# Kernel tuning notes

Hardware: AMD Instinct MI355X
Metric: run time of the kernel (lower is better)

Reference implementation:

```python
import jax, jax.numpy as jnp
import numpy as np
from jax.ops import segment_sum

N_NODES = 50000
N_EDGES = 800000
IN_DIM, HID_DIM, OUT_DIM = 128, 256, 128


def _glorot(key, shape):
    lim = np.sqrt(6.0 / (shape[0] + shape[1]))
    return jax.random.uniform(key, shape, jnp.float32, -lim, lim)


def setup_inputs() -> dict:
    key = jax.random.key(0)
    ks = jax.random.split(key, 4)
    x = jax.random.normal(ks[0], (N_NODES, IN_DIM), jnp.float32)
    edge_index = jax.random.randint(ks[1], (2, N_EDGES), 0, N_NODES, jnp.int64)
    W1 = _glorot(ks[2], (IN_DIM, HID_DIM))
    b1 = jnp.zeros((HID_DIM,), jnp.float32)
    W2 = _glorot(ks[3], (HID_DIM, OUT_DIM))
    b2 = jnp.zeros((OUT_DIM,), jnp.float32)
    return {"x": x, "edge_index": edge_index, "W1": W1, "b1": b1, "W2": W2, "b2": b2}


def gcn_conv(x, W, b, src, dst, n_nodes):
    # PyG GCNConv: x' = D^{-1/2} (A + I) D^{-1/2} (x W) + b
    h = x @ W  # [N, F_out]
    deg = segment_sum(jnp.ones_like(src, dtype=h.dtype), dst, num_segments=n_nodes) + 1.0  # +1 self loop
    dinv = jax.lax.rsqrt(deg)  # [N]
    norm = dinv[src] * dinv[dst]  # per-edge norm [E]
    msg = h[src] * norm[:, None]  # [E, F_out]
    agg = segment_sum(msg, dst, num_segments=n_nodes)
    agg = agg + h * (dinv * dinv)[:, None]  # self-loop term: norm_ii = dinv_i^2
    return agg + b


def reference(x, edge_index, W1, b1, W2, b2):
    src, dst = edge_index[0], edge_index[1]
    h = gcn_conv(x, W1, b1, src, dst, N_NODES)
    h = jax.nn.relu(h)
    out = gcn_conv(h, W2, b2, src, dst, N_NODES)
    return out
```

## Files before the change

### kernel.cpp

```cpp
#include <hip/hip_runtime.h>

#define N_NODES 50000
#define N_EDGES 800000
#define IN_DIM  128
#define HID_DIM 256
#define OUT_DIM 128
#define BUCKET_CAP 64
#define NCOARSE 196
#define CHUNK 4000
#define NBLK1 200
#define SEGCAP 64
#define HLD 264
#define GROWS 64

typedef __attribute__((ext_vector_type(8))) short short8;
typedef __attribute__((ext_vector_type(4))) float f32x4;

__device__ inline ushort f2b(float f) {
    union { float f; unsigned u; } v; v.f = f;
    return (ushort)((v.u + 0x7FFFu + ((v.u >> 16) & 1u)) >> 16);
}
__device__ inline float b2f(ushort h) {
    union { unsigned u; float f; } v; v.u = ((unsigned)h) << 16;
    return v.f;
}
__device__ inline float2 u2f2(unsigned u) {
    float2 r; r.x = b2f((ushort)(u & 0xFFFFu)); r.y = b2f((ushort)(u >> 16)); return r;
}
__device__ inline unsigned f2u2(float a, float b) {
    return (unsigned)f2b(a) | ((unsigned)f2b(b) << 16);
}
__device__ inline void fma8(float2* acc, uint4 u, float n) {
    float2 v0 = u2f2(u.x), v1 = u2f2(u.y), v2 = u2f2(u.z), v3 = u2f2(u.w);
    acc[0].x += v0.x * n; acc[0].y += v0.y * n;
    acc[1].x += v1.x * n; acc[1].y += v1.y * n;
    acc[2].x += v2.x * n; acc[2].y += v2.y * n;
    acc[3].x += v3.x * n; acc[3].y += v3.y * n;
}


__global__ __launch_bounds__(256) void prep_kernel(const float* __restrict__ x,
                                                   const float* __restrict__ W1,
                                                   const float* __restrict__ W2,
                                                   const int* __restrict__ src,
                                                   const int* __restrict__ dst,
                                                   ushort* __restrict__ xb,
                                                   ushort* __restrict__ w1t,
                                                   ushort* __restrict__ w2t,
                                                   int* __restrict__ bcnt,
                                                   int* __restrict__ binbuf) {
    __shared__ int vals[CHUNK];
    __shared__ ushort lpos[CHUNK];
    __shared__ unsigned char lbin[CHUNK];
    __shared__ int hist[NCOARSE];
    const int b = blockIdx.x;
    const int t = threadIdx.x;
    if (b < 6250) {
        int i = b * 256 + t;
        float4 v = ((const float4*)x)[i];
        ushort4 o; o.x = f2b(v.x); o.y = f2b(v.y); o.z = f2b(v.z); o.w = f2b(v.w);
        ((ushort4*)xb)[i] = o;
    } else if (b < 6506) {
        int i = (b - 6250) * 256 + t;
        if (i < 32768) {
            int n = i >> 7, k = i & 127;
            w1t[i] = f2b(W1[k * HID_DIM + n]);
        } else {
            int j = i - 32768;
            int n = j >> 8, k = j & 255;
            w2t[j] = f2b(W2[k * OUT_DIM + n]);
        }
    } else {
        const int blk = b - 6506;
        const int e0 = blk * CHUNK;
        for (int i = t; i < NCOARSE; i += 256) hist[i] = 0;
        __syncthreads();
        for (int i = t; i < CHUNK; i += 256) {
            int s = src[e0 + i], d = dst[e0 + i];
            int bin = d >> 8;
            vals[i] = (s << 8) | (d & 255);
            lbin[i] = (unsigned char)bin;
            lpos[i] = (ushort)atomicAdd(&hist[bin], 1);
        }
        __syncthreads();
        for (int i = t; i < NCOARSE; i += 256) {
            int h = hist[i]; if (h > SEGCAP) h = SEGCAP;
            bcnt[i * NBLK1 + blk] = h;
        }
        for (int i = t; i < CHUNK; i += 256) {
            int bin = lbin[i];
            int p = lpos[i];
            if (p < SEGCAP) binbuf[((size_t)bin * NBLK1 + blk) * SEGCAP + p] = vals[i];
        }
    }
}


__global__ __launch_bounds__(256) void binpass2_kernel(const int* __restrict__ bcnt,
                                                       const int* __restrict__ binbuf,
                                                       int* __restrict__ cnt,
                                                       float* __restrict__ dinv,
                                                       int* __restrict__ bucket) {
    __shared__ int lcnt[256];
    __shared__ int lm[NBLK1];
    __shared__ int lbuck[256 * BUCKET_CAP];
    const int bin = blockIdx.x;
    const int t = threadIdx.x;
    lcnt[t] = 0;
    if (t < NBLK1) lm[t] = bcnt[bin * NBLK1 + t];
    __syncthreads();
    const int* bb = binbuf + (size_t)bin * NBLK1 * SEGCAP;
    for (int f = t; f < NBLK1 * SEGCAP; f += 256) {
        int blk = f >> 6;
        int sl = f & 63;
        if (sl < lm[blk]) {
            int v = bb[f];
            int dl = v & 255;
            int pos = atomicAdd(&lcnt[dl], 1);
            if (pos < BUCKET_CAP) lbuck[dl * BUCKET_CAP + pos] = v >> 8;
        }
    }
    __syncthreads();
    const int node0 = bin * 256;
    int node = node0 + t;
    if (node < N_NODES) {
        int c = lcnt[t] > BUCKET_CAP ? BUCKET_CAP : lcnt[t];
        cnt[node] = c;
        dinv[node] = rsqrtf((float)c + 1.0f);
    }
    int nvalid = N_NODES - node0; if (nvalid > 256) nvalid = 256;
    if (nvalid <= 0) return;
    int total4 = (nvalid * BUCKET_CAP) >> 2;
    int4* d4 = (int4*)(bucket + (size_t)node0 * BUCKET_CAP);
    const int4* s4 = (const int4*)lbuck;
    for (int j = t; j < total4; j += 256) d4[j] = s4[j];
}


__global__ __launch_bounds__(256) void gather0_kernel(const int* __restrict__ cnt,
                                                      const int* __restrict__ bucket,
                                                      const float* __restrict__ dinv,
                                                      const ushort* __restrict__ xb,
                                                      ushort* __restrict__ aggxb) {
    const int w = blockIdx.x * 4 + (threadIdx.x >> 6);
    const int lane = threadIdx.x & 63;
    const int grp = lane >> 4, sub = lane & 15;
    const int n = cnt[w];
    const float dd = dinv[w];
    int sv = 0; float nv = 0.f;
    if (lane < n) { sv = bucket[w * BUCKET_CAP + lane]; nv = dinv[sv] * dd; }

    float2 acc[4];
    if (grp == 0) {
        uint4 su = ((const uint4*)(xb + (size_t)w * IN_DIM))[sub];
        float sd = dd * dd;
        acc[0] = u2f2(su.x); acc[1] = u2f2(su.y); acc[2] = u2f2(su.z); acc[3] = u2f2(su.w);
#pragma unroll
        for (int j = 0; j < 4; ++j) { acc[j].x *= sd; acc[j].y *= sd; }
    } else {
#pragma unroll
        for (int j = 0; j < 4; ++j) acc[j] = {0.f, 0.f};
    }

    const int nr = (n + 15) & ~15;
    for (int i = 0; i < nr; i += 16) {
        int s0 = __shfl(sv, i + grp),      s1 = __shfl(sv, i + 4 + grp);
        int s2 = __shfl(sv, i + 8 + grp),  s3 = __shfl(sv, i + 12 + grp);
        float n0 = __shfl(nv, i + grp),     n1 = __shfl(nv, i + 4 + grp);
        float n2 = __shfl(nv, i + 8 + grp), n3 = __shfl(nv, i + 12 + grp);
        uint4 u0 = ((const uint4*)(xb + (size_t)s0 * IN_DIM))[sub];
        uint4 u1 = ((const uint4*)(xb + (size_t)s1 * IN_DIM))[sub];
        uint4 u2 = ((const uint4*)(xb + (size_t)s2 * IN_DIM))[sub];
        uint4 u3 = ((const uint4*)(xb + (size_t)s3 * IN_DIM))[sub];
        fma8(acc, u0, n0); fma8(acc, u1, n1); fma8(acc, u2, n2); fma8(acc, u3, n3);
    }
#pragma unroll
    for (int j = 0; j < 4; ++j) {
        acc[j].x += __shfl_down(acc[j].x, 32); acc[j].y += __shfl_down(acc[j].y, 32);
        acc[j].x += __shfl_down(acc[j].x, 16); acc[j].y += __shfl_down(acc[j].y, 16);
    }
    if (lane < 16) {
        uint4 o = {f2u2(acc[0].x, acc[0].y), f2u2(acc[1].x, acc[1].y),
                   f2u2(acc[2].x, acc[2].y), f2u2(acc[3].x, acc[3].y)};
        ((uint4*)(aggxb + (size_t)w * IN_DIM))[sub] = o;
    }
}


__global__ __launch_bounds__(256, 2) void gemm12_mfma(const ushort* __restrict__ aggxb,
                                                      const ushort* __restrict__ w1t,
                                                      const float* __restrict__ b1,
                                                      const ushort* __restrict__ w2t,
                                                      ushort* __restrict__ h2b) {
    __shared__ ushort Hs[GROWS * HLD];
    const int row0 = blockIdx.x * GROWS;
    const int wv = threadIdx.x >> 6;
    const int lane = threadIdx.x & 63;
    const int l15 = lane & 15, q = lane >> 4;

    short8 bf1[16];
#pragma unroll
    for (int kb = 0; kb < 4; ++kb)
#pragma unroll
        for (int t = 0; t < 4; ++t) {
            int col = wv * 64 + t * 16 + l15;
            bf1[kb * 4 + t] = *(const short8*)(w1t + (size_t)col * IN_DIM + kb * 32 + q * 8);
        }
    short8 af[4][4];
#pragma unroll
    for (int sub = 0; sub < 4; ++sub) {
        int ar = row0 + sub * 16 + l15;
        if (ar >= N_NODES) ar = N_NODES - 1;
        const ushort* ab = aggxb + (size_t)ar * IN_DIM + q * 8;
#pragma unroll
        for (int kb = 0; kb < 4; ++kb) af[sub][kb] = *(const short8*)(ab + kb * 32);
    }
    f32x4 acc1[4][4] = {};
#pragma unroll
    for (int sub = 0; sub < 4; ++sub)
#pragma unroll
        for (int kb = 0; kb < 4; ++kb)
#pragma unroll
            for (int t = 0; t < 4; ++t)
                acc1[sub][t] = __builtin_amdgcn_mfma_f32_16x16x32_bf16(
                    af[sub][kb], bf1[kb * 4 + t], acc1[sub][t], 0, 0, 0);
#pragma unroll
    for (int t = 0; t < 4; ++t) {
        int col = wv * 64 + t * 16 + l15;
        float bias = b1[col];
#pragma unroll
        for (int sub = 0; sub < 4; ++sub)
#pragma unroll
            for (int r = 0; r < 4; ++r) {
                int row = sub * 16 + q * 4 + r;
                float v = acc1[sub][t][r] + bias;
                Hs[row * HLD + col] = f2b(v > 0.f ? v : 0.f);
            }
    }
    __syncthreads();

    short8 bf2[16];
#pragma unroll
    for (int kb = 0; kb < 8; ++kb)
#pragma unroll
        for (int t = 0; t < 2; ++t) {
            int col = wv * 32 + t * 16 + l15;
            bf2[kb * 2 + t] = *(const short8*)(w2t + (size_t)col * HID_DIM + kb * 32 + q * 8);
        }
    f32x4 acc2[4][2] = {};
#pragma unroll
    for (int sub = 0; sub < 4; ++sub) {
        const ushort* hb = Hs + (sub * 16 + l15) * HLD + q * 8;
#pragma unroll
        for (int kb = 0; kb < 8; ++kb) {
            short8 a = *(const short8*)(hb + kb * 32);
#pragma unroll
            for (int t = 0; t < 2; ++t)
                acc2[sub][t] = __builtin_amdgcn_mfma_f32_16x16x32_bf16(
                    a, bf2[kb * 2 + t], acc2[sub][t], 0, 0, 0);
        }
    }
#pragma unroll
    for (int sub = 0; sub < 4; ++sub)
#pragma unroll
        for (int t = 0; t < 2; ++t) {
            int col = wv * 32 + t * 16 + l15;
#pragma unroll
            for (int r = 0; r < 4; ++r) {
                int row = row0 + sub * 16 + q * 4 + r;
                if (row < N_NODES)
                    h2b[(size_t)row * OUT_DIM + col] = f2b(acc2[sub][t][r]);
            }
        }
}


__global__ __launch_bounds__(256) void gather2_kernel(const int* __restrict__ cnt,
                                                      const int* __restrict__ bucket,
                                                      const float* __restrict__ dinv,
                                                      const ushort* __restrict__ h2b,
                                                      const float* __restrict__ b2,
                                                      float* __restrict__ out) {
    const int w = blockIdx.x * 4 + (threadIdx.x >> 6);
    const int lane = threadIdx.x & 63;
    const int grp = lane >> 4, sub = lane & 15;
    const int n = cnt[w];
    const float dd = dinv[w];
    int sv = 0; float nv = 0.f;
    if (lane < n) { sv = bucket[w * BUCKET_CAP + lane]; nv = dinv[sv] * dd; }

    float2 acc[4];
    if (grp == 0) {
        uint4 su = ((const uint4*)(h2b + (size_t)w * OUT_DIM))[sub];
        float sd = dd * dd;
        acc[0] = u2f2(su.x); acc[1] = u2f2(su.y); acc[2] = u2f2(su.z); acc[3] = u2f2(su.w);
#pragma unroll
        for (int j = 0; j < 4; ++j) { acc[j].x *= sd; acc[j].y *= sd; }
    } else {
#pragma unroll
        for (int j = 0; j < 4; ++j) acc[j] = {0.f, 0.f};
    }

    const int nr = (n + 15) & ~15;
    for (int i = 0; i < nr; i += 16) {
        int s0 = __shfl(sv, i + grp),      s1 = __shfl(sv, i + 4 + grp);
        int s2 = __shfl(sv, i + 8 + grp),  s3 = __shfl(sv, i + 12 + grp);
        float n0 = __shfl(nv, i + grp),     n1 = __shfl(nv, i + 4 + grp);
        float n2 = __shfl(nv, i + 8 + grp), n3 = __shfl(nv, i + 12 + grp);
        uint4 u0 = ((const uint4*)(h2b + (size_t)s0 * OUT_DIM))[sub];
        uint4 u1 = ((const uint4*)(h2b + (size_t)s1 * OUT_DIM))[sub];
        uint4 u2 = ((const uint4*)(h2b + (size_t)s2 * OUT_DIM))[sub];
        uint4 u3 = ((const uint4*)(h2b + (size_t)s3 * OUT_DIM))[sub];
        fma8(acc, u0, n0); fma8(acc, u1, n1); fma8(acc, u2, n2); fma8(acc, u3, n3);
    }
#pragma unroll
    for (int j = 0; j < 4; ++j) {
        acc[j].x += __shfl_down(acc[j].x, 32); acc[j].y += __shfl_down(acc[j].y, 32);
        acc[j].x += __shfl_down(acc[j].x, 16); acc[j].y += __shfl_down(acc[j].y, 16);
    }
    if (lane < 16) {
        const float4* bp = (const float4*)b2;
        float4 b0 = bp[sub * 2], b1v = bp[sub * 2 + 1];
        float4 o0 = {acc[0].x + b0.x, acc[0].y + b0.y, acc[1].x + b0.z, acc[1].y + b0.w};
        float4 o1 = {acc[2].x + b1v.x, acc[2].y + b1v.y, acc[3].x + b1v.z, acc[3].y + b1v.w};
        float4* op = (float4*)(out + (size_t)w * OUT_DIM);
        op[sub * 2] = o0;
        op[sub * 2 + 1] = o1;
    }
}

extern "C" void kernel_launch(void* const* d_in, const int* in_sizes, int n_in,
                              void* d_out, int out_size, void* d_ws, size_t ws_size,
                              hipStream_t stream) {
    const float* x  = (const float*)d_in[0];
    const int*   ei = (const int*)d_in[1];
    const float* W1 = (const float*)d_in[2];
    const float* b1 = (const float*)d_in[3];
    const float* W2 = (const float*)d_in[4];
    const float* b2 = (const float*)d_in[5];
    float* out = (float*)d_out;

    const int* src = ei;
    const int* dst = ei + N_EDGES;

    char* ws = (char*)d_ws;
    int*    bcnt   = (int*)(ws);
    int*    cnt    = (int*)(ws + 160000);
    float*  dinv   = (float*)(ws + 360000);
    int*    bucket = (int*)(ws + 560000);
    int*    binbuf = (int*)(ws + 13360000);
    ushort* xb     = (ushort*)(ws + 23395200);
    ushort* w1t    = (ushort*)(ws + 36195200);
    ushort* w2t    = (ushort*)(ws + 36260736);
    ushort* aggxb  = (ushort*)(ws + 36326272);
    ushort* h2b    = (ushort*)(ws + 49126272);

    prep_kernel<<<6706, 256, 0, stream>>>(x, W1, W2, src, dst, xb, w1t, w2t, bcnt, binbuf);
    binpass2_kernel<<<NCOARSE, 256, 0, stream>>>(bcnt, binbuf, cnt, dinv, bucket);

    gather0_kernel<<<N_NODES / 4, 256, 0, stream>>>(cnt, bucket, dinv, xb, aggxb);
    gemm12_mfma<<<(N_NODES + GROWS - 1) / GROWS, 256, 0, stream>>>(aggxb, w1t, b1, w2t, h2b);

    gather2_kernel<<<N_NODES / 4, 256, 0, stream>>>(cnt, bucket, dinv, h2b, b2, out);
}
```

Baseline: 215.5 us.

## Split gather kernels across feature halves to double wave parallelism

Both gather kernels now assign each node to two waves, each handling one 64-column half of the 128-wide bf16 feature row, with blocks interleaved so both halves of a node group run in adjacent blocks. The point is more waves in flight and more memory-level parallelism on the random row gathers. In exchange, neighbor index and norm loads plus the shuffles are duplicated per half, and each lane's load is 8 bytes instead of 16. Paired blocks may share the same rows in cache.

```diff
diff --git a/kernel.cpp b/kernel.cpp
--- a/kernel.cpp
+++ b/kernel.cpp
@@ -30,12 +30,10 @@
 __device__ inline unsigned f2u2(float a, float b) {
     return (unsigned)f2b(a) | ((unsigned)f2b(b) << 16);
 }
-__device__ inline void fma8(float2* acc, uint4 u, float n) {
-    float2 v0 = u2f2(u.x), v1 = u2f2(u.y), v2 = u2f2(u.z), v3 = u2f2(u.w);
+__device__ inline void fma4h(float2* acc, uint2 u, float n) {
+    float2 v0 = u2f2(u.x), v1 = u2f2(u.y);
     acc[0].x += v0.x * n; acc[0].y += v0.y * n;
     acc[1].x += v1.x * n; acc[1].y += v1.y * n;
-    acc[2].x += v2.x * n; acc[2].y += v2.y * n;
-    acc[3].x += v3.x * n; acc[3].y += v3.y * n;
 }
 
 
@@ -142,24 +140,26 @@
                                                       const float* __restrict__ dinv,
                                                       const ushort* __restrict__ xb,
                                                       ushort* __restrict__ aggxb) {
-    const int w = blockIdx.x * 4 + (threadIdx.x >> 6);
+    const int b = blockIdx.x;
+    const int wv = threadIdx.x >> 6;
     const int lane = threadIdx.x & 63;
+    const int half = (b & 7) >> 2;
+    const int node = ((b >> 3) * 4 + (b & 3)) * 4 + wv;
     const int grp = lane >> 4, sub = lane & 15;
-    const int n = cnt[w];
-    const float dd = dinv[w];
+    const int n = cnt[node];
+    const float dd = dinv[node];
     int sv = 0; float nv = 0.f;
-    if (lane < n) { sv = bucket[w * BUCKET_CAP + lane]; nv = dinv[sv] * dd; }
-
-    float2 acc[4];
+    if (lane < n) { sv = bucket[node * BUCKET_CAP + lane]; nv = dinv[sv] * dd; }
+
+    const ushort* base = xb + half * 64;
+    float2 acc[2];
     if (grp == 0) {
-        uint4 su = ((const uint4*)(xb + (size_t)w * IN_DIM))[sub];
+        uint2 su = ((const uint2*)(base + (size_t)node * IN_DIM))[sub];
         float sd = dd * dd;
-        acc[0] = u2f2(su.x); acc[1] = u2f2(su.y); acc[2] = u2f2(su.z); acc[3] = u2f2(su.w);
-#pragma unroll
-        for (int j = 0; j < 4; ++j) { acc[j].x *= sd; acc[j].y *= sd; }
+        acc[0] = u2f2(su.x); acc[1] = u2f2(su.y);
+        acc[0].x *= sd; acc[0].y *= sd; acc[1].x *= sd; acc[1].y *= sd;
     } else {
-#pragma unroll
-        for (int j = 0; j < 4; ++j) acc[j] = {0.f, 0.f};
+        acc[0] = {0.f, 0.f}; acc[1] = {0.f, 0.f};
     }
 
     const int nr = (n + 15) & ~15;
@@ -168,21 +168,20 @@
         int s2 = __shfl(sv, i + 8 + grp),  s3 = __shfl(sv, i + 12 + grp);
         float n0 = __shfl(nv, i + grp),     n1 = __shfl(nv, i + 4 + grp);
         float n2 = __shfl(nv, i + 8 + grp), n3 = __shfl(nv, i + 12 + grp);
-        uint4 u0 = ((const uint4*)(xb + (size_t)s0 * IN_DIM))[sub];
-        uint4 u1 = ((const uint4*)(xb + (size_t)s1 * IN_DIM))[sub];
-        uint4 u2 = ((const uint4*)(xb + (size_t)s2 * IN_DIM))[sub];
-        uint4 u3 = ((const uint4*)(xb + (size_t)s3 * IN_DIM))[sub];
-        fma8(acc, u0, n0); fma8(acc, u1, n1); fma8(acc, u2, n2); fma8(acc, u3, n3);
-    }
-#pragma unroll
-    for (int j = 0; j < 4; ++j) {
+        uint2 u0 = ((const uint2*)(base + (size_t)s0 * IN_DIM))[sub];
+        uint2 u1 = ((const uint2*)(base + (size_t)s1 * IN_DIM))[sub];
+        uint2 u2 = ((const uint2*)(base + (size_t)s2 * IN_DIM))[sub];
+        uint2 u3 = ((const uint2*)(base + (size_t)s3 * IN_DIM))[sub];
+        fma4h(acc, u0, n0); fma4h(acc, u1, n1); fma4h(acc, u2, n2); fma4h(acc, u3, n3);
+    }
+#pragma unroll
+    for (int j = 0; j < 2; ++j) {
         acc[j].x += __shfl_down(acc[j].x, 32); acc[j].y += __shfl_down(acc[j].y, 32);
         acc[j].x += __shfl_down(acc[j].x, 16); acc[j].y += __shfl_down(acc[j].y, 16);
     }
     if (lane < 16) {
-        uint4 o = {f2u2(acc[0].x, acc[0].y), f2u2(acc[1].x, acc[1].y),
-                   f2u2(acc[2].x, acc[2].y), f2u2(acc[3].x, acc[3].y)};
-        ((uint4*)(aggxb + (size_t)w * IN_DIM))[sub] = o;
+        uint2 o = {f2u2(acc[0].x, acc[0].y), f2u2(acc[1].x, acc[1].y)};
+        ((uint2*)(aggxb + (size_t)node * IN_DIM + half * 64))[sub] = o;
     }
 }
 
@@ -281,24 +280,26 @@
                                                       const ushort* __restrict__ h2b,
                                                       const float* __restrict__ b2,
                                                       float* __restrict__ out) {
-    const int w = blockIdx.x * 4 + (threadIdx.x >> 6);
+    const int b = blockIdx.x;
+    const int wv = threadIdx.x >> 6;
     const int lane = threadIdx.x & 63;
+    const int half = (b & 7) >> 2;
+    const int node = ((b >> 3) * 4 + (b & 3)) * 4 + wv;
     const int grp = lane >> 4, sub = lane & 15;
-    const int n = cnt[w];
-    const float dd = dinv[w];
+    const int n = cnt[node];
+    const float dd = dinv[node];
     int sv = 0; float nv = 0.f;
-    if (lane < n) { sv = bucket[w * BUCKET_CAP + lane]; nv = dinv[sv] * dd; }
-
-    float2 acc[4];
+    if (lane < n) { sv = bucket[node * BUCKET_CAP + lane]; nv = dinv[sv] * dd; }
+
+    const ushort* base = h2b + half * 64;
+    float2 acc[2];
     if (grp == 0) {
-        uint4 su = ((const uint4*)(h2b + (size_t)w * OUT_DIM))[sub];
+        uint2 su = ((const uint2*)(base + (size_t)node * OUT_DIM))[sub];
         float sd = dd * dd;
-        acc[0] = u2f2(su.x); acc[1] = u2f2(su.y); acc[2] = u2f2(su.z); acc[3] = u2f2(su.w);
-#pragma unroll
-        for (int j = 0; j < 4; ++j) { acc[j].x *= sd; acc[j].y *= sd; }
+        acc[0] = u2f2(su.x); acc[1] = u2f2(su.y);
+        acc[0].x *= sd; acc[0].y *= sd; acc[1].x *= sd; acc[1].y *= sd;
     } else {
-#pragma unroll
-        for (int j = 0; j < 4; ++j) acc[j] = {0.f, 0.f};
+        acc[0] = {0.f, 0.f}; acc[1] = {0.f, 0.f};
     }
 
     const int nr = (n + 15) & ~15;
@@ -307,25 +308,21 @@
         int s2 = __shfl(sv, i + 8 + grp),  s3 = __shfl(sv, i + 12 + grp);
         float n0 = __shfl(nv, i + grp),     n1 = __shfl(nv, i + 4 + grp);
         float n2 = __shfl(nv, i + 8 + grp), n3 = __shfl(nv, i + 12 + grp);
-        uint4 u0 = ((const uint4*)(h2b + (size_t)s0 * OUT_DIM))[sub];
-        uint4 u1 = ((const uint4*)(h2b + (size_t)s1 * OUT_DIM))[sub];
-        uint4 u2 = ((const uint4*)(h2b + (size_t)s2 * OUT_DIM))[sub];
-        uint4 u3 = ((const uint4*)(h2b + (size_t)s3 * OUT_DIM))[sub];
-        fma8(acc, u0, n0); fma8(acc, u1, n1); fma8(acc, u2, n2); fma8(acc, u3, n3);
-    }
-#pragma unroll
-    for (int j = 0; j < 4; ++j) {
+        uint2 u0 = ((const uint2*)(base + (size_t)s0 * OUT_DIM))[sub];
+        uint2 u1 = ((const uint2*)(base + (size_t)s1 * OUT_DIM))[sub];
+        uint2 u2 = ((const uint2*)(base + (size_t)s2 * OUT_DIM))[sub];
+        uint2 u3 = ((const uint2*)(base + (size_t)s3 * OUT_DIM))[sub];
+        fma4h(acc, u0, n0); fma4h(acc, u1, n1); fma4h(acc, u2, n2); fma4h(acc, u3, n3);
+    }
+#pragma unroll
+    for (int j = 0; j < 2; ++j) {
         acc[j].x += __shfl_down(acc[j].x, 32); acc[j].y += __shfl_down(acc[j].y, 32);
         acc[j].x += __shfl_down(acc[j].x, 16); acc[j].y += __shfl_down(acc[j].y, 16);
     }
     if (lane < 16) {
-        const float4* bp = (const float4*)b2;
-        float4 b0 = bp[sub * 2], b1v = bp[sub * 2 + 1];
-        float4 o0 = {acc[0].x + b0.x, acc[0].y + b0.y, acc[1].x + b0.z, acc[1].y + b0.w};
-        float4 o1 = {acc[2].x + b1v.x, acc[2].y + b1v.y, acc[3].x + b1v.z, acc[3].y + b1v.w};
-        float4* op = (float4*)(out + (size_t)w * OUT_DIM);
-        op[sub * 2] = o0;
-        op[sub * 2 + 1] = o1;
+        float4 bb = ((const float4*)b2)[half * 16 + sub];
+        float4 o = {acc[0].x + bb.x, acc[0].y + bb.y, acc[1].x + bb.z, acc[1].y + bb.w};
+        ((float4*)(out + (size_t)node * OUT_DIM + half * 64))[sub] = o;
     }
 }
 
@@ -358,8 +355,8 @@
     prep_kernel<<<6706, 256, 0, stream>>>(x, W1, W2, src, dst, xb, w1t, w2t, bcnt, binbuf);
     binpass2_kernel<<<NCOARSE, 256, 0, stream>>>(bcnt, binbuf, cnt, dinv, bucket);
 
-    gather0_kernel<<<N_NODES / 4, 256, 0, stream>>>(cnt, bucket, dinv, xb, aggxb);
+    gather0_kernel<<<N_NODES / 2, 256, 0, stream>>>(cnt, bucket, dinv, xb, aggxb);
     gemm12_mfma<<<(N_NODES + GROWS - 1) / GROWS, 256, 0, stream>>>(aggxb, w1t, b1, w2t, h2b);
 
-    gather2_kernel<<<N_NODES / 4, 256, 0, stream>>>(cnt, bucket, dinv, h2b, b2, out);
-}
+    gather2_kernel<<<N_NODES / 2, 256, 0, stream>>>(cnt, bucket, dinv, h2b, b2, out);
+}
```

After: 236.3 us. 1.1x slower.

## Split gather feature dimension across two blocks and cache per-edge norms

Applied to the files above, without the earlier changes.

Each gather kernel now splits the 128-wide feature row into two 64-column halves handled by separate blocks, doubling the grid and halving per-wave work. Blocks are interleaved so both halves of a node group run close together. gather0 also stores the per-edge normalisation into a new workspace buffer, which gather2 reads instead of redoing the dependent dinv[src] lookup. The cost is duplicated index and count loads per half, an extra reduction shuffle step, and extra writes for the norm buffer.

```diff
diff --git a/kernel.cpp b/kernel.cpp
--- a/kernel.cpp
+++ b/kernel.cpp
@@ -141,18 +141,24 @@
                                                       const int* __restrict__ bucket,
                                                       const float* __restrict__ dinv,
                                                       const ushort* __restrict__ xb,
-                                                      ushort* __restrict__ aggxb) {
-    const int w = blockIdx.x * 4 + (threadIdx.x >> 6);
+                                                      ushort* __restrict__ aggxb,
+                                                      float* __restrict__ normbuf) {
+    const int b = blockIdx.x;
+    const int wv = threadIdx.x >> 6;
     const int lane = threadIdx.x & 63;
-    const int grp = lane >> 4, sub = lane & 15;
-    const int n = cnt[w];
-    const float dd = dinv[w];
+    const int half = (b & 7) >> 2;
+    const int node = ((b >> 3) * 4 + (b & 3)) * 4 + wv;
+    const int grp = lane >> 3, sub = lane & 7;
+    const int n = cnt[node];
+    const float dd = dinv[node];
     int sv = 0; float nv = 0.f;
-    if (lane < n) { sv = bucket[w * BUCKET_CAP + lane]; nv = dinv[sv] * dd; }
-
+    if (lane < n) { sv = bucket[node * BUCKET_CAP + lane]; nv = dinv[sv] * dd; }
+    if (half == 0 && lane < n) normbuf[node * BUCKET_CAP + lane] = nv;
+
+    const ushort* base = xb + half * 64;
     float2 acc[4];
     if (grp == 0) {
-        uint4 su = ((const uint4*)(xb + (size_t)w * IN_DIM))[sub];
+        uint4 su = ((const uint4*)(base + (size_t)node * IN_DIM))[sub];
         float sd = dd * dd;
         acc[0] = u2f2(su.x); acc[1] = u2f2(su.y); acc[2] = u2f2(su.z); acc[3] = u2f2(su.w);
 #pragma unroll
@@ -164,25 +170,22 @@
 
     const int nr = (n + 15) & ~15;
     for (int i = 0; i < nr; i += 16) {
-        int s0 = __shfl(sv, i + grp),      s1 = __shfl(sv, i + 4 + grp);
-        int s2 = __shfl(sv, i + 8 + grp),  s3 = __shfl(sv, i + 12 + grp);
-        float n0 = __shfl(nv, i + grp),     n1 = __shfl(nv, i + 4 + grp);
-        float n2 = __shfl(nv, i + 8 + grp), n3 = __shfl(nv, i + 12 + grp);
-        uint4 u0 = ((const uint4*)(xb + (size_t)s0 * IN_DIM))[sub];
-        uint4 u1 = ((const uint4*)(xb + (size_t)s1 * IN_DIM))[sub];
-        uint4 u2 = ((const uint4*)(xb + (size_t)s2 * IN_DIM))[sub];
-        uint4 u3 = ((const uint4*)(xb + (size_t)s3 * IN_DIM))[sub];
-        fma8(acc, u0, n0); fma8(acc, u1, n1); fma8(acc, u2, n2); fma8(acc, u3, n3);
+        int s0 = __shfl(sv, i + grp), s1 = __shfl(sv, i + 8 + grp);
+        float n0 = __shfl(nv, i + grp), n1 = __shfl(nv, i + 8 + grp);
+        uint4 u0 = ((const uint4*)(base + (size_t)s0 * IN_DIM))[sub];
+        uint4 u1 = ((const uint4*)(base + (size_t)s1 * IN_DIM))[sub];
+        fma8(acc, u0, n0); fma8(acc, u1, n1);
     }
 #pragma unroll
     for (int j = 0; j < 4; ++j) {
         acc[j].x += __shfl_down(acc[j].x, 32); acc[j].y += __shfl_down(acc[j].y, 32);
         acc[j].x += __shfl_down(acc[j].x, 16); acc[j].y += __shfl_down(acc[j].y, 16);
-    }
-    if (lane < 16) {
+        acc[j].x += __shfl_down(acc[j].x, 8);  acc[j].y += __shfl_down(acc[j].y, 8);
+    }
+    if (lane < 8) {
         uint4 o = {f2u2(acc[0].x, acc[0].y), f2u2(acc[1].x, acc[1].y),
                    f2u2(acc[2].x, acc[2].y), f2u2(acc[3].x, acc[3].y)};
-        ((uint4*)(aggxb + (size_t)w * IN_DIM))[sub] = o;
+        ((uint4*)(aggxb + (size_t)node * IN_DIM + half * 64))[sub] = o;
     }
 }
 
@@ -278,20 +281,28 @@
 __global__ __launch_bounds__(256) void gather2_kernel(const int* __restrict__ cnt,
                                                       const int* __restrict__ bucket,
                                                       const float* __restrict__ dinv,
+                                                      const float* __restrict__ normbuf,
                                                       const ushort* __restrict__ h2b,
                                                       const float* __restrict__ b2,
                                                       float* __restrict__ out) {
-    const int w = blockIdx.x * 4 + (threadIdx.x >> 6);
+    const int b = blockIdx.x;
+    const int wv = threadIdx.x >> 6;
     const int lane = threadIdx.x & 63;
-    const int grp = lane >> 4, sub = lane & 15;
-    const int n = cnt[w];
-    const float dd = dinv[w];
+    const int half = (b & 7) >> 2;
+    const int node = ((b >> 3) * 4 + (b & 3)) * 4 + wv;
+    const int grp = lane >> 3, sub = lane & 7;
+    const int n = cnt[node];
+    const float dd = dinv[node];
     int sv = 0; float nv = 0.f;
-    if (lane < n) { sv = bucket[w * BUCKET_CAP + lane]; nv = dinv[sv] * dd; }
-
+    if (lane < n) {
+        sv = bucket[node * BUCKET_CAP + lane];
+        nv = normbuf[node * BUCKET_CAP + lane];
+    }
+
+    const ushort* base = h2b + half * 64;
     float2 acc[4];
     if (grp == 0) {
-        uint4 su = ((const uint4*)(h2b + (size_t)w * OUT_DIM))[sub];
+        uint4 su = ((const uint4*)(base + (size_t)node * OUT_DIM))[sub];
         float sd = dd * dd;
         acc[0] = u2f2(su.x); acc[1] = u2f2(su.y); acc[2] = u2f2(su.z); acc[3] = u2f2(su.w);
 #pragma unroll
@@ -303,27 +314,24 @@
 
     const int nr = (n + 15) & ~15;
     for (int i = 0; i < nr; i += 16) {
-        int s0 = __shfl(sv, i + grp),      s1 = __shfl(sv, i + 4 + grp);
-        int s2 = __shfl(sv, i + 8 + grp),  s3 = __shfl(sv, i + 12 + grp);
-        float n0 = __shfl(nv, i + grp),     n1 = __shfl(nv, i + 4 + grp);
-        float n2 = __shfl(nv, i + 8 + grp), n3 = __shfl(nv, i + 12 + grp);
-        uint4 u0 = ((const uint4*)(h2b + (size_t)s0 * OUT_DIM))[sub];
-        uint4 u1 = ((const uint4*)(h2b + (size_t)s1 * OUT_DIM))[sub];
-        uint4 u2 = ((const uint4*)(h2b + (size_t)s2 * OUT_DIM))[sub];
-        uint4 u3 = ((const uint4*)(h2b + (size_t)s3 * OUT_DIM))[sub];
-        fma8(acc, u0, n0); fma8(acc, u1, n1); fma8(acc, u2, n2); fma8(acc, u3, n3);
+        int s0 = __shfl(sv, i + grp), s1 = __shfl(sv, i + 8 + grp);
+        float n0 = __shfl(nv, i + grp), n1 = __shfl(nv, i + 8 + grp);
+        uint4 u0 = ((const uint4*)(base + (size_t)s0 * OUT_DIM))[sub];
+        uint4 u1 = ((const uint4*)(base + (size_t)s1 * OUT_DIM))[sub];
+        fma8(acc, u0, n0); fma8(acc, u1, n1);
     }
 #pragma unroll
     for (int j = 0; j < 4; ++j) {
         acc[j].x += __shfl_down(acc[j].x, 32); acc[j].y += __shfl_down(acc[j].y, 32);
         acc[j].x += __shfl_down(acc[j].x, 16); acc[j].y += __shfl_down(acc[j].y, 16);
-    }
-    if (lane < 16) {
+        acc[j].x += __shfl_down(acc[j].x, 8);  acc[j].y += __shfl_down(acc[j].y, 8);
+    }
+    if (lane < 8) {
         const float4* bp = (const float4*)b2;
-        float4 b0 = bp[sub * 2], b1v = bp[sub * 2 + 1];
-        float4 o0 = {acc[0].x + b0.x, acc[0].y + b0.y, acc[1].x + b0.z, acc[1].y + b0.w};
-        float4 o1 = {acc[2].x + b1v.x, acc[2].y + b1v.y, acc[3].x + b1v.z, acc[3].y + b1v.w};
-        float4* op = (float4*)(out + (size_t)w * OUT_DIM);
+        float4 ba = bp[half * 16 + sub * 2], bb = bp[half * 16 + sub * 2 + 1];
+        float4 o0 = {acc[0].x + ba.x, acc[0].y + ba.y, acc[1].x + ba.z, acc[1].y + ba.w};
+        float4 o1 = {acc[2].x + bb.x, acc[2].y + bb.y, acc[3].x + bb.z, acc[3].y + bb.w};
+        float4* op = (float4*)(out + (size_t)node * OUT_DIM + half * 64);
         op[sub * 2] = o0;
         op[sub * 2 + 1] = o1;
     }
@@ -344,22 +352,23 @@
     const int* dst = ei + N_EDGES;
 
     char* ws = (char*)d_ws;
-    int*    bcnt   = (int*)(ws);
-    int*    cnt    = (int*)(ws + 160000);
-    float*  dinv   = (float*)(ws + 360000);
-    int*    bucket = (int*)(ws + 560000);
-    int*    binbuf = (int*)(ws + 13360000);
-    ushort* xb     = (ushort*)(ws + 23395200);
-    ushort* w1t    = (ushort*)(ws + 36195200);
-    ushort* w2t    = (ushort*)(ws + 36260736);
-    ushort* aggxb  = (ushort*)(ws + 36326272);
-    ushort* h2b    = (ushort*)(ws + 49126272);
+    int*    bcnt    = (int*)(ws);
+    int*    cnt     = (int*)(ws + 160000);
+    float*  dinv    = (float*)(ws + 360000);
+    int*    bucket  = (int*)(ws + 560000);
+    int*    binbuf  = (int*)(ws + 13360000);
+    ushort* xb      = (ushort*)(ws + 23395200);
+    ushort* w1t     = (ushort*)(ws + 36195200);
+    ushort* w2t     = (ushort*)(ws + 36260736);
+    ushort* aggxb   = (ushort*)(ws + 36326272);
+    ushort* h2b     = (ushort*)(ws + 49126272);
+    float*  normbuf = (float*)(ws + 61926272);
 
     prep_kernel<<<6706, 256, 0, stream>>>(x, W1, W2, src, dst, xb, w1t, w2t, bcnt, binbuf);
     binpass2_kernel<<<NCOARSE, 256, 0, stream>>>(bcnt, binbuf, cnt, dinv, bucket);
 
-    gather0_kernel<<<N_NODES / 4, 256, 0, stream>>>(cnt, bucket, dinv, xb, aggxb);
+    gather0_kernel<<<N_NODES / 2, 256, 0, stream>>>(cnt, bucket, dinv, xb, aggxb, normbuf);
     gemm12_mfma<<<(N_NODES + GROWS - 1) / GROWS, 256, 0, stream>>>(aggxb, w1t, b1, w2t, h2b);
 
-    gather2_kernel<<<N_NODES / 4, 256, 0, stream>>>(cnt, bucket, dinv, h2b, b2, out);
-}
+    gather2_kernel<<<N_NODES / 2, 256, 0, stream>>>(cnt, bucket, dinv, normbuf, h2b, b2, out);
+}
```

After: 234.2 us. +8.7%, slower.
